# Optimization experiments

Hardware: AMD Instinct MI355X
Metric: run time of the kernel (lower is better)

## Reference

```python
import jax, jax.numpy as jnp
import numpy as np

EPS = 1e-9


def setup_inputs() -> dict:
    key = jax.random.key(0)
    k1, k2, k3, k4 = jax.random.split(key, 4)
    B, N = 8192, 256
    T, Q = 4096, 64
    reprs = jax.random.normal(k1, (B, N), dtype=jnp.float32)
    memory = jax.random.normal(k2, (T, Q, N), dtype=jnp.float32)
    # memory bank rows are kept unit-norm by the module's renormalization
    memory = memory / (jnp.linalg.norm(memory, axis=-1, keepdims=True) + EPS)
    alpha = jax.random.uniform(k3, (Q, 1), dtype=jnp.float32)
    track_idxs = jax.random.randint(k4, (B,), 0, T, dtype=jnp.int64)
    return {"reprs": reprs, "memory": memory, "alpha": alpha, "track_idxs": track_idxs}


def reference(reprs, memory, alpha, track_idxs):
    # Vectorized equivalent of MemoryBank.update (init != 'zeros' branch):
    # per track t present in track_idxs, per slot q:
    #   b* = argmin_{b: track_idxs[b]==t} <memory[t,q], reprs[b]>   (first occurrence)
    #   m  = alpha[q] * memory[t,q] + (1-alpha[q]) * reprs[b*]
    #   memory[t,q] = m / (||m|| + eps)
    B, N = reprs.shape
    T, Q, _ = memory.shape
    tid = track_idxs.astype(jnp.int32)

    # similarity of each detection against its own track's Q slots: [B, Q]
    sim = jnp.einsum('bqn,bn->bq', memory[tid], reprs)

    # segment-min over detections of each track -> [T, Q]
    min_val = jnp.full((T, Q), jnp.inf, dtype=sim.dtype).at[tid].min(sim)
    # first detection index achieving the min (matches torch argmin tie-break)
    b_idx = jnp.arange(B, dtype=jnp.int32)[:, None]                 # [B, 1]
    cand = jnp.where(sim == min_val[tid], b_idx, B)                 # [B, Q]
    chosen = jnp.full((T, Q), B, dtype=jnp.int32).at[tid].min(cand)  # [T, Q]

    present = chosen[:, 0] < B                                       # [T]
    sel = reprs[jnp.minimum(chosen, B - 1)]                          # [T, Q, N]

    upd = memory * alpha + sel * (1.0 - alpha)                       # alpha: [Q,1]
    upd = upd / (jnp.linalg.norm(upd, axis=-1, keepdims=True) + EPS)
    return jnp.where(present[:, None, None], upd, memory)
```

## Files before the change

kernel.cpp:

```cpp
#include <hip/hip_runtime.h>
#include <stdint.h>

#define B_DET 8192
#define N_DIM 256
#define T_TRK 4096
#define Q_SLOT 64
#define MAXD   64
#define CHUNK  8
#define EPSF   1e-9f

typedef unsigned long long ull;

__device__ __forceinline__ uint32_t f32_key(float f) {
    uint32_t u = __float_as_uint(f);
    return (u & 0x80000000u) ? ~u : (u | 0x80000000u);
}
__device__ __forceinline__ float key_inv(uint32_t k) {
    uint32_t u = (k & 0x80000000u) ? (k ^ 0x80000000u) : ~k;
    return __uint_as_float(u);
}

__global__ __launch_bounds__(256)
void build_lists(const int* __restrict__ track_idxs,
                 int* __restrict__ cnt, int* __restrict__ list) {
    const int b = blockIdx.x * 256 + threadIdx.x;
    const int t = track_idxs[b];
    const int slot = atomicAdd(&cnt[t], 1);
    if (slot < MAXD) list[t * MAXD + slot] = b;
}

__global__ __launch_bounds__(256, 4)
void fused_update(const float* __restrict__ reprs,
                  const float* __restrict__ memory,
                  const float* __restrict__ alpha,
                  const int* __restrict__ cnt,
                  const int* __restrict__ list,
                  float* __restrict__ out) {
    const int t    = blockIdx.x >> 1;
    const int half = blockIdx.x & 1;
    const int wave = threadIdx.x >> 6;
    const int lane = threadIdx.x & 63;
    const int g    = lane >> 4;
    const int cidx = lane & 15;
    const int qbase = half * 32 + wave * 8;
    const size_t tbase = (size_t)t * Q_SLOT * N_DIM;

    int D = cnt[t];
    if (D == 0) {
        const size_t rbase = tbase + (size_t)qbase * N_DIM;
        float4 mm[8];
        #pragma unroll
        for (int s = 0; s < 8; ++s)
            mm[s] = reinterpret_cast<const float4*>(memory + rbase + (size_t)s * N_DIM)[lane];
        #pragma unroll
        for (int s = 0; s < 8; ++s)
            reinterpret_cast<float4*>(out + rbase + (size_t)s * N_DIM)[lane] = mm[s];
        return;
    }
    if (D > MAXD) D = MAXD;
    const int nchunks = (D + CHUNK - 1) / CHUNK;

    float4 m[2][4];
    #pragma unroll
    for (int i = 0; i < 2; ++i) {
        const float* rp = memory + tbase + (size_t)(qbase + i * 4 + g) * N_DIM;
        #pragma unroll
        for (int c = 0; c < 4; ++c)
            m[i][c] = reinterpret_cast<const float4*>(rp)[cidx + c * 16];
    }

    __shared__ float rsh[CHUNK][N_DIM];

    ull   best[2] = { ~0ULL, ~0ULL };
    float bRn2[2] = { 0.0f, 0.0f };

    for (int c = 0; c < nchunks; ++c) {
        __syncthreads();
        const int dlim = min(CHUNK, D - c * CHUNK);
        for (int dd = 0; dd < dlim; ++dd) {
            const int b = list[t * MAXD + c * CHUNK + dd];
            rsh[dd][threadIdx.x] = reprs[(size_t)b * N_DIM + threadIdx.x];
        }
        __syncthreads();

        for (int dd = 0; dd < dlim; ++dd) {
            const int dg = c * CHUNK + dd;
            const int b  = list[t * MAXD + dg];

            float4 rc[4];
            #pragma unroll
            for (int cc = 0; cc < 4; ++cc)
                rc[cc] = reinterpret_cast<const float4*>(&rsh[dd][0])[cidx + cc * 16];

            float p0 = 0.0f, p1 = 0.0f, rr = 0.0f;
            #pragma unroll
            for (int cc = 0; cc < 4; ++cc) {
                p0 += m[0][cc].x * rc[cc].x + m[0][cc].y * rc[cc].y
                    + m[0][cc].z * rc[cc].z + m[0][cc].w * rc[cc].w;
                p1 += m[1][cc].x * rc[cc].x + m[1][cc].y * rc[cc].y
                    + m[1][cc].z * rc[cc].z + m[1][cc].w * rc[cc].w;
                rr += rc[cc].x * rc[cc].x + rc[cc].y * rc[cc].y
                    + rc[cc].z * rc[cc].z + rc[cc].w * rc[cc].w;
            }
            #pragma unroll
            for (int o = 8; o >= 1; o >>= 1) {
                p0 += __shfl_xor(p0, o, 64);
                p1 += __shfl_xor(p1, o, 64);
                rr += __shfl_xor(rr, o, 64);
            }

            const uint32_t bd = ((uint32_t)b << 6) | (uint32_t)dg;
            const ull k0 = ((ull)f32_key(p0) << 32) | bd;
            const ull k1 = ((ull)f32_key(p1) << 32) | bd;
            if (k0 < best[0]) { best[0] = k0; bRn2[0] = rr; }
            if (k1 < best[1]) { best[1] = k1; bRn2[1] = rr; }
        }
    }

    const bool single = (nchunks == 1);

    #pragma unroll
    for (int i = 0; i < 2; ++i) {
        const int q = qbase + i * 4 + g;
        const uint32_t lo = (uint32_t)best[i];
        const int   bsel = (int)(lo >> 6);
        const int   dsel = (int)(lo & 63);
        const float dot  = key_inv((uint32_t)(best[i] >> 32));
        const float a    = alpha[q];
        const float na   = 1.0f - a;

        float4 rc[4];
        if (single) {
            #pragma unroll
            for (int cc = 0; cc < 4; ++cc)
                rc[cc] = reinterpret_cast<const float4*>(&rsh[dsel][0])[cidx + cc * 16];
        } else {
            const float* rp = reprs + (size_t)bsel * N_DIM;
            #pragma unroll
            for (int cc = 0; cc < 4; ++cc)
                rc[cc] = reinterpret_cast<const float4*>(rp)[cidx + cc * 16];
        }

        const float nrm2 = a * a + na * na * bRn2[i] + 2.0f * a * na * dot;
        const float sc = 1.0f / (sqrtf(nrm2) + EPSF);

        float* op = out + tbase + (size_t)q * N_DIM;
        #pragma unroll
        for (int cc = 0; cc < 4; ++cc) {
            float4 u;
            u.x = (a * m[i][cc].x + na * rc[cc].x) * sc;
            u.y = (a * m[i][cc].y + na * rc[cc].y) * sc;
            u.z = (a * m[i][cc].z + na * rc[cc].z) * sc;
            u.w = (a * m[i][cc].w + na * rc[cc].w) * sc;
            reinterpret_cast<float4*>(op)[cidx + cc * 16] = u;
        }
    }
}

extern "C" void kernel_launch(void* const* d_in, const int* in_sizes, int n_in,
                              void* d_out, int out_size, void* d_ws, size_t ws_size,
                              hipStream_t stream) {
    const float* reprs      = (const float*)d_in[0];
    const float* memory     = (const float*)d_in[1];
    const float* alpha      = (const float*)d_in[2];
    const int*   track_idxs = (const int*)d_in[3];
    float*       out        = (float*)d_out;

    int* cnt  = (int*)d_ws;
    int* list = (int*)((char*)d_ws + T_TRK * sizeof(int));

    hipMemsetAsync(cnt, 0, T_TRK * sizeof(int), stream);
    build_lists<<<B_DET / 256, 256, 0, stream>>>(track_idxs, cnt, list);
    fused_update<<<T_TRK * 2, 256, 0, stream>>>(reprs, memory, alpha, cnt, list, out);
}
```

Baseline: 112.6 us.

## Replace shared-memory chunk staging with register double-buffered direct loads of reprs

Drops the shared-memory staging of detection vectors and the per-chunk __syncthreads. Each wave now loads reprs rows straight into registers and prefetches the next row while computing the current one. The final blend always re-reads the chosen row from global memory. The launch-bounds occupancy hint is removed too. The aim is to cut barrier stalls and LDS traffic, at the cost of redundant global/L2 loads across waves and possibly more register pressure.

```diff
diff --git a/kernel.cpp b/kernel.cpp
--- a/kernel.cpp
+++ b/kernel.cpp
@@ -6,7 +6,6 @@
 #define T_TRK 4096
 #define Q_SLOT 64
 #define MAXD   64
-#define CHUNK  8
 #define EPSF   1e-9f
 
 typedef unsigned long long ull;
@@ -29,7 +28,7 @@
     if (slot < MAXD) list[t * MAXD + slot] = b;
 }
 
-__global__ __launch_bounds__(256, 4)
+__global__ __launch_bounds__(256)
 void fused_update(const float* __restrict__ reprs,
                   const float* __restrict__ memory,
                   const float* __restrict__ alpha,
@@ -37,12 +36,11 @@
                   const int* __restrict__ list,
                   float* __restrict__ out) {
     const int t    = blockIdx.x >> 1;
-    const int half = blockIdx.x & 1;
     const int wave = threadIdx.x >> 6;
     const int lane = threadIdx.x & 63;
     const int g    = lane >> 4;
     const int cidx = lane & 15;
-    const int qbase = half * 32 + wave * 8;
+    const int qbase = (blockIdx.x & 1) * 32 + wave * 8;
     const size_t tbase = (size_t)t * Q_SLOT * N_DIM;
 
     int D = cnt[t];
@@ -58,7 +56,6 @@
         return;
     }
     if (D > MAXD) D = MAXD;
-    const int nchunks = (D + CHUNK - 1) / CHUNK;
 
     float4 m[2][4];
     #pragma unroll
@@ -69,89 +66,78 @@
             m[i][c] = reinterpret_cast<const float4*>(rp)[cidx + c * 16];
     }
 
-    __shared__ float rsh[CHUNK][N_DIM];
-
     ull   best[2] = { ~0ULL, ~0ULL };
     float bRn2[2] = { 0.0f, 0.0f };
 
-    for (int c = 0; c < nchunks; ++c) {
-        __syncthreads();
-        const int dlim = min(CHUNK, D - c * CHUNK);
-        for (int dd = 0; dd < dlim; ++dd) {
-            const int b = list[t * MAXD + c * CHUNK + dd];
-            rsh[dd][threadIdx.x] = reprs[(size_t)b * N_DIM + threadIdx.x];
-        }
-        __syncthreads();
+    int b_cur = list[t * MAXD];
+    float4 rc[4];
+    {
+        const float* rp = reprs + (size_t)b_cur * N_DIM;
+        #pragma unroll
+        for (int cc = 0; cc < 4; ++cc)
+            rc[cc] = reinterpret_cast<const float4*>(rp)[cidx + cc * 16];
+    }
 
-        for (int dd = 0; dd < dlim; ++dd) {
-            const int dg = c * CHUNK + dd;
-            const int b  = list[t * MAXD + dg];
-
-            float4 rc[4];
+    for (int d = 0; d < D; ++d) {
+        int b_nxt = 0;
+        float4 rn[4];
+        if (d + 1 < D) {
+            b_nxt = list[t * MAXD + d + 1];
+            const float* rp = reprs + (size_t)b_nxt * N_DIM;
             #pragma unroll
             for (int cc = 0; cc < 4; ++cc)
-                rc[cc] = reinterpret_cast<const float4*>(&rsh[dd][0])[cidx + cc * 16];
+                rn[cc] = reinterpret_cast<const float4*>(rp)[cidx + cc * 16];
+        }
 
-            float p0 = 0.0f, p1 = 0.0f, rr = 0.0f;
-            #pragma unroll
-            for (int cc = 0; cc < 4; ++cc) {
-                p0 += m[0][cc].x * rc[cc].x + m[0][cc].y * rc[cc].y
-                    + m[0][cc].z * rc[cc].z + m[0][cc].w * rc[cc].w;
-                p1 += m[1][cc].x * rc[cc].x + m[1][cc].y * rc[cc].y
-                    + m[1][cc].z * rc[cc].z + m[1][cc].w * rc[cc].w;
-                rr += rc[cc].x * rc[cc].x + rc[cc].y * rc[cc].y
-                    + rc[cc].z * rc[cc].z + rc[cc].w * rc[cc].w;
-            }
-            #pragma unroll
-            for (int o = 8; o >= 1; o >>= 1) {
-                p0 += __shfl_xor(p0, o, 64);
-                p1 += __shfl_xor(p1, o, 64);
-                rr += __shfl_xor(rr, o, 64);
-            }
+        float p0 = 0.0f, p1 = 0.0f, rr = 0.0f;
+        #pragma unroll
+        for (int cc = 0; cc < 4; ++cc) {
+            p0 += m[0][cc].x * rc[cc].x + m[0][cc].y * rc[cc].y
+                + m[0][cc].z * rc[cc].z + m[0][cc].w * rc[cc].w;
+            p1 += m[1][cc].x * rc[cc].x + m[1][cc].y * rc[cc].y
+                + m[1][cc].z * rc[cc].z + m[1][cc].w * rc[cc].w;
+            rr += rc[cc].x * rc[cc].x + rc[cc].y * rc[cc].y
+                + rc[cc].z * rc[cc].z + rc[cc].w * rc[cc].w;
+        }
+        #pragma unroll
+        for (int o = 8; o >= 1; o >>= 1) {
+            p0 += __shfl_xor(p0, o, 64);
+            p1 += __shfl_xor(p1, o, 64);
+            rr += __shfl_xor(rr, o, 64);
+        }
 
-            const uint32_t bd = ((uint32_t)b << 6) | (uint32_t)dg;
-            const ull k0 = ((ull)f32_key(p0) << 32) | bd;
-            const ull k1 = ((ull)f32_key(p1) << 32) | bd;
-            if (k0 < best[0]) { best[0] = k0; bRn2[0] = rr; }
-            if (k1 < best[1]) { best[1] = k1; bRn2[1] = rr; }
-        }
+        const uint32_t bd = ((uint32_t)b_cur << 6) | (uint32_t)d;
+        const ull k0 = ((ull)f32_key(p0) << 32) | bd;
+        const ull k1 = ((ull)f32_key(p1) << 32) | bd;
+        if (k0 < best[0]) { best[0] = k0; bRn2[0] = rr; }
+        if (k1 < best[1]) { best[1] = k1; bRn2[1] = rr; }
+
+        b_cur = b_nxt;
+        #pragma unroll
+        for (int cc = 0; cc < 4; ++cc) rc[cc] = rn[cc];
     }
-
-    const bool single = (nchunks == 1);
 
     #pragma unroll
     for (int i = 0; i < 2; ++i) {
         const int q = qbase + i * 4 + g;
-        const uint32_t lo = (uint32_t)best[i];
-        const int   bsel = (int)(lo >> 6);
-        const int   dsel = (int)(lo & 63);
+        const int   bsel = (int)(((uint32_t)best[i]) >> 6);
         const float dot  = key_inv((uint32_t)(best[i] >> 32));
         const float a    = alpha[q];
         const float na   = 1.0f - a;
 
-        float4 rc[4];
-        if (single) {
-            #pragma unroll
-            for (int cc = 0; cc < 4; ++cc)
-                rc[cc] = reinterpret_cast<const float4*>(&rsh[dsel][0])[cidx + cc * 16];
-        } else {
-            const float* rp = reprs + (size_t)bsel * N_DIM;
-            #pragma unroll
-            for (int cc = 0; cc < 4; ++cc)
-                rc[cc] = reinterpret_cast<const float4*>(rp)[cidx + cc * 16];
-        }
-
+        const float* rp = reprs + (size_t)bsel * N_DIM;
         const float nrm2 = a * a + na * na * bRn2[i] + 2.0f * a * na * dot;
         const float sc = 1.0f / (sqrtf(nrm2) + EPSF);
 
         float* op = out + tbase + (size_t)q * N_DIM;
         #pragma unroll
         for (int cc = 0; cc < 4; ++cc) {
+            const float4 r = reinterpret_cast<const float4*>(rp)[cidx + cc * 16];
             float4 u;
-            u.x = (a * m[i][cc].x + na * rc[cc].x) * sc;
-            u.y = (a * m[i][cc].y + na * rc[cc].y) * sc;
-            u.z = (a * m[i][cc].z + na * rc[cc].z) * sc;
-            u.w = (a * m[i][cc].w + na * rc[cc].w) * sc;
+            u.x = (a * m[i][cc].x + na * r.x) * sc;
+            u.y = (a * m[i][cc].y + na * r.y) * sc;
+            u.z = (a * m[i][cc].z + na * r.z) * sc;
+            u.w = (a * m[i][cc].w + na * r.w) * sc;
             reinterpret_cast<float4*>(op)[cidx + cc * 16] = u;
         }
     }
```

After: 111.5 us. No clear change (-0.9%).
